# Kernel optimization log

Measured on AMD Instinct MI355X. Metric: run time of the kernel, lower is better.

Reference implementation:

```python
import jax, jax.numpy as jnp
import numpy as np

C, H, W = 96, 128, 128
D_EMB, D_HID = 2, 16


def setup_inputs() -> dict:
    key = jax.random.key(0)
    k1, k2, k3, k4, k5 = jax.random.split(key, 5)
    x = jax.random.normal(k1, (16, C, H, W), dtype=jnp.float32)
    # MLP params: Linear(d_emb, d_hidden) -> ReLU -> Linear(d_hidden, hidden_size)
    W1 = jax.random.normal(k2, (D_EMB, D_HID), dtype=jnp.float32) / np.sqrt(D_EMB)
    b1 = jax.random.normal(k3, (D_HID,), dtype=jnp.float32) * 0.01
    W2 = jax.random.normal(k4, (D_HID, C), dtype=jnp.float32) / np.sqrt(D_HID)
    b2 = jax.random.normal(k5, (C,), dtype=jnp.float32) * 0.01
    return {"x": x, "W1": W1, "b1": b1, "W2": W2, "b2": b2}


def reference(x, W1, b1, W2, b2):
    B, Cc, Hh, Ww = x.shape
    # positional grid (y/H, x/W) in [0,1], shape [H, W, 2]
    gy, gx = jnp.meshgrid(jnp.linspace(0.0, 1.0, Hh), jnp.linspace(0.0, 1.0, Ww), indexing="ij")
    pe = jnp.stack([gy, gx], axis=-1).reshape(-1, 2)  # [H*W, 2]
    hid = jax.nn.relu(pe @ W1 + b1)                   # [H*W, d_hidden]
    k = (hid @ W2 + b2).T.reshape(Cc, Hh, Ww)         # [C, H, W]
    fh, fw = 2 * Hh, 2 * Ww
    k_f = jnp.fft.rfft2(k, s=(fh, fw))                # [C, fh, fw//2+1]
    x_f = jnp.fft.rfft2(x, s=(fh, fw))                # [B, C, fh, fw//2+1]
    # torch: rfft2 norm='backward' (unscaled) + irfft2 norm='forward' (unscaled)
    # => net factor of fh*fw, replicated faithfully via norm='forward'.
    y = jnp.fft.irfft2(x_f * k_f[None], s=(fh, fw), norm="forward")
    y = y[..., :Hh, :Ww]
    return y + x  # residual=True, gelu=False
```

## Files before the change

kernel.cpp:

```cpp
#include <hip/hip_runtime.h>
#include <hip/hip_fp16.h>

#define TWO_PI 6.283185307179586f
#define PI_F   3.14159265358979f

#define HH 128
#define WW 128
#define FN 256
#define NF 129
#define CC 96
#define BB 16

#define SCL_DN 0.0009765625f
#define SCL_UP 1024.0f

typedef unsigned int uint2v __attribute__((ext_vector_type(2)));
typedef __fp16 half2v __attribute__((ext_vector_type(2)));

__device__ __forceinline__ float2 cmul(float2 a, float2 b){
  return make_float2(a.x*b.x - a.y*b.y, a.x*b.y + a.y*b.x);
}
__device__ __forceinline__ float2 cmulc(float2 a, float2 b){
  return make_float2(a.x*b.x + a.y*b.y, a.x*b.y - a.y*b.x);
}
__device__ __forceinline__ float2 cadd(float2 a, float2 b){ return make_float2(a.x+b.x, a.y+b.y); }
__device__ __forceinline__ float2 csub(float2 a, float2 b){ return make_float2(a.x-b.x, a.y-b.y); }
__device__ __forceinline__ float2 shflx(float2 v, int m){
  float2 r; r.x = __shfl_xor(v.x, m, 64); r.y = __shfl_xor(v.y, m, 64); return r;
}
__device__ __forceinline__ float2 shfli(float2 v, int idx){
  float2 r; r.x = __shfl(v.x, idx, 64); r.y = __shfl(v.y, idx, 64); return r;
}
__device__ __forceinline__ unsigned short f2h(float v){ return __half_as_ushort(__float2half(v)); }
__device__ __forceinline__ float h2f(unsigned short u){ return __half2float(__ushort_as_half(u)); }
__device__ __forceinline__ unsigned pkh2(float a, float b){
  union { half2v h; unsigned u; } cv;
  cv.h = __builtin_amdgcn_cvt_pkrtz(a, b);
  return cv.u;
}
__device__ __forceinline__ float h2lo(unsigned u){ return h2f((unsigned short)(u & 0xffffu)); }
__device__ __forceinline__ float h2hi(unsigned u){ return h2f((unsigned short)(u >> 16)); }

__device__ __forceinline__ void swp32(float2 v, float2& lo, float2& hi){
  uint2v rx = __builtin_amdgcn_permlane32_swap(__float_as_uint(v.x), __float_as_uint(v.x), false, false);
  uint2v ry = __builtin_amdgcn_permlane32_swap(__float_as_uint(v.y), __float_as_uint(v.y), false, false);
  lo = make_float2(__uint_as_float(rx[0]), __uint_as_float(ry[0]));
  hi = make_float2(__uint_as_float(rx[1]), __uint_as_float(ry[1]));
}
__device__ __forceinline__ void swp16(float2 v, float2& lo, float2& hi){
  uint2v rx = __builtin_amdgcn_permlane16_swap(__float_as_uint(v.x), __float_as_uint(v.x), false, false);
  uint2v ry = __builtin_amdgcn_permlane16_swap(__float_as_uint(v.y), __float_as_uint(v.y), false, false);
  lo = make_float2(__uint_as_float(rx[0]), __uint_as_float(ry[0]));
  hi = make_float2(__uint_as_float(rx[1]), __uint_as_float(ry[1]));
}
template<int CTRL>
__device__ __forceinline__ float2 dppx(float2 v){
  float2 r;
  r.x = __uint_as_float((unsigned)__builtin_amdgcn_update_dpp(0, (int)__float_as_uint(v.x), CTRL, 0xF, 0xF, true));
  r.y = __uint_as_float((unsigned)__builtin_amdgcn_update_dpp(0, (int)__float_as_uint(v.y), CTRL, 0xF, 0xF, true));
  return r;
}
#define DPP_XOR1 0xB1
#define DPP_XOR2 0x4E

struct Tw {
  float2 w128a, w128b, w64;
  float2 wc[5];
  float2 wf[5];
  float  sg[5];
  float  sg1;
};

__device__ __forceinline__ void tw_init(Tw& t, int l){
  float s, c;
  sincosf(-TWO_PI * (float)l * (1.0f/256.0f), &s, &c);
  t.w128a = make_float2(c, s);
  t.w128b = make_float2(s, -c);
  t.w64   = make_float2(c*c - s*s, 2.0f*c*s);
  const int hs[5] = {32,16,8,4,2};
#pragma unroll
  for (int i = 0; i < 5; ++i){
    int h = hs[i];
    float ang = -PI_F * (float)(l & (h-1)) / (float)h;
    sincosf(ang, &s, &c);
    t.wc[i] = make_float2(c, s);
    bool dn = (l & h) != 0;
    t.wf[i] = dn ? t.wc[i] : make_float2(1.0f, 0.0f);
    t.sg[i] = dn ? -1.0f : 1.0f;
  }
  t.sg1 = (l & 1) ? -1.0f : 1.0f;
}

#define FX_OTHER(X, OTHER, SG, WF) { \
  float2 o_ = OTHER; float2 s_; \
  s_.x = fmaf(SG, X.x, o_.x); s_.y = fmaf(SG, X.y, o_.y); \
  X = cmul(WF, s_); }
#define FX_LOHI(X, SWPF, SG, WF) { \
  float2 lo_, hi_, s_; SWPF(X, lo_, hi_); \
  s_.x = fmaf(SG, hi_.x, lo_.x); s_.y = fmaf(SG, hi_.y, lo_.y); \
  X = cmul(WF, s_); }
#define IX_LOHI(X, SWPF, SG, WC) { \
  float2 lo_, hi_, m_; SWPF(X, lo_, hi_); \
  m_ = cmulc(WC, hi_); \
  X.x = fmaf(SG, m_.x, lo_.x); X.y = fmaf(SG, m_.y, lo_.y); }
#define IX_OTHER(X, OTHER, UP, SG, WC) { \
  float2 o_ = OTHER; \
  float2 A_ = UP ? X : o_; \
  float2 B_ = UP ? o_ : X; \
  float2 m_ = cmulc(WC, B_); \
  X.x = fmaf(SG, m_.x, A_.x); X.y = fmaf(SG, m_.y, A_.y); }

__device__ __forceinline__ void fft256_fwd_padded(float2& x0, float2& x1,
                                                  float2& x2, float2& x3,
                                                  const Tw& t, int l){
  x2 = cmul(x0, t.w128a);
  x3 = cmul(x1, t.w128b);
  float2 a = x0, b = x1;
  x0 = cadd(a, b); x1 = cmul(csub(a, b), t.w64);
  a = x2; b = x3;
  x2 = cadd(a, b); x3 = cmul(csub(a, b), t.w64);
  FX_LOHI(x0, swp32, t.sg[0], t.wf[0]);
  FX_LOHI(x1, swp32, t.sg[0], t.wf[0]);
  FX_LOHI(x2, swp32, t.sg[0], t.wf[0]);
  FX_LOHI(x3, swp32, t.sg[0], t.wf[0]);
  FX_LOHI(x0, swp16, t.sg[1], t.wf[1]);
  FX_LOHI(x1, swp16, t.sg[1], t.wf[1]);
  FX_LOHI(x2, swp16, t.sg[1], t.wf[1]);
  FX_LOHI(x3, swp16, t.sg[1], t.wf[1]);
  FX_OTHER(x0, shflx(x0, 8), t.sg[2], t.wf[2]);
  FX_OTHER(x1, shflx(x1, 8), t.sg[2], t.wf[2]);
  FX_OTHER(x2, shflx(x2, 8), t.sg[2], t.wf[2]);
  FX_OTHER(x3, shflx(x3, 8), t.sg[2], t.wf[2]);
  FX_OTHER(x0, shflx(x0, 4), t.sg[3], t.wf[3]);
  FX_OTHER(x1, shflx(x1, 4), t.sg[3], t.wf[3]);
  FX_OTHER(x2, shflx(x2, 4), t.sg[3], t.wf[3]);
  FX_OTHER(x3, shflx(x3, 4), t.sg[3], t.wf[3]);
  FX_OTHER(x0, dppx<DPP_XOR2>(x0), t.sg[4], t.wf[4]);
  FX_OTHER(x1, dppx<DPP_XOR2>(x1), t.sg[4], t.wf[4]);
  FX_OTHER(x2, dppx<DPP_XOR2>(x2), t.sg[4], t.wf[4]);
  FX_OTHER(x3, dppx<DPP_XOR2>(x3), t.sg[4], t.wf[4]);
  {
    float2 o;
    o = dppx<DPP_XOR1>(x0); x0.x = fmaf(t.sg1, x0.x, o.x); x0.y = fmaf(t.sg1, x0.y, o.y);
    o = dppx<DPP_XOR1>(x1); x1.x = fmaf(t.sg1, x1.x, o.x); x1.y = fmaf(t.sg1, x1.y, o.y);
    o = dppx<DPP_XOR1>(x2); x2.x = fmaf(t.sg1, x2.x, o.x); x2.y = fmaf(t.sg1, x2.y, o.y);
    o = dppx<DPP_XOR1>(x3); x3.x = fmaf(t.sg1, x3.x, o.x); x3.y = fmaf(t.sg1, x3.y, o.y);
  }
}

__device__ __forceinline__ void fft256_inv_crop(float2& x0, float2& x1,
                                                float2& x2, float2& x3,
                                                const Tw& t, int l){
  {
    float2 o;
    o = dppx<DPP_XOR1>(x0); x0.x = fmaf(t.sg1, x0.x, o.x); x0.y = fmaf(t.sg1, x0.y, o.y);
    o = dppx<DPP_XOR1>(x1); x1.x = fmaf(t.sg1, x1.x, o.x); x1.y = fmaf(t.sg1, x1.y, o.y);
    o = dppx<DPP_XOR1>(x2); x2.x = fmaf(t.sg1, x2.x, o.x); x2.y = fmaf(t.sg1, x2.y, o.y);
    o = dppx<DPP_XOR1>(x3); x3.x = fmaf(t.sg1, x3.x, o.x); x3.y = fmaf(t.sg1, x3.y, o.y);
  }
  {
    bool up = (l & 2) == 0;
    IX_OTHER(x0, dppx<DPP_XOR2>(x0), up, t.sg[4], t.wc[4]);
    IX_OTHER(x1, dppx<DPP_XOR2>(x1), up, t.sg[4], t.wc[4]);
    IX_OTHER(x2, dppx<DPP_XOR2>(x2), up, t.sg[4], t.wc[4]);
    IX_OTHER(x3, dppx<DPP_XOR2>(x3), up, t.sg[4], t.wc[4]);
  }
  {
    bool up = (l & 4) == 0;
    IX_OTHER(x0, shflx(x0, 4), up, t.sg[3], t.wc[3]);
    IX_OTHER(x1, shflx(x1, 4), up, t.sg[3], t.wc[3]);
    IX_OTHER(x2, shflx(x2, 4), up, t.sg[3], t.wc[3]);
    IX_OTHER(x3, shflx(x3, 4), up, t.sg[3], t.wc[3]);
  }
  {
    bool up = (l & 8) == 0;
    IX_OTHER(x0, shflx(x0, 8), up, t.sg[2], t.wc[2]);
    IX_OTHER(x1, shflx(x1, 8), up, t.sg[2], t.wc[2]);
    IX_OTHER(x2, shflx(x2, 8), up, t.sg[2], t.wc[2]);
    IX_OTHER(x3, shflx(x3, 8), up, t.sg[2], t.wc[2]);
  }
  IX_LOHI(x0, swp16, t.sg[1], t.wc[1]);
  IX_LOHI(x1, swp16, t.sg[1], t.wc[1]);
  IX_LOHI(x2, swp16, t.sg[1], t.wc[1]);
  IX_LOHI(x3, swp16, t.sg[1], t.wc[1]);
  IX_LOHI(x0, swp32, t.sg[0], t.wc[0]);
  IX_LOHI(x1, swp32, t.sg[0], t.wc[0]);
  IX_LOHI(x2, swp32, t.sg[0], t.wc[0]);
  IX_LOHI(x3, swp32, t.sg[0], t.wc[0]);
  {
    float2 w = make_float2(t.w64.x, -t.w64.y);
    float2 t0 = cmul(w, x1); x1 = csub(x0, t0); x0 = cadd(x0, t0);
    float2 t1 = cmul(w, x3); x3 = csub(x2, t1); x2 = cadd(x2, t1);
  }
  {
    float2 wa = make_float2(t.w128a.x, -t.w128a.y);
    float2 wb = make_float2(t.w128b.x, -t.w128b.y);
    x0 = cadd(x0, cmul(wa, x2));
    x1 = cadd(x1, cmul(wb, x3));
  }
}


__global__ __launch_bounds__(512) void kprep_col(const float* __restrict__ W1,
                                                 const float* __restrict__ b1,
                                                 const float* __restrict__ W2,
                                                 const float* __restrict__ b2,
                                                 float2* __restrict__ Khat){
  __shared__ float sRe[NF*65];
  __shared__ float sIm[NF*65];
  const int S = 65;
  int t = threadIdx.x, l = t & 63, w = t >> 6;
  int c  = blockIdx.x >> 1;
  int q0B = (blockIdx.x & 1) * 64;
  Tw tw; tw_init(tw, l);
  int r6 = __brev((unsigned)l) >> 26;
  int l63 = l ^ 63;
  int p0 = __brev((unsigned)((64 - r6) & 63)) >> 26;

  float w1y[16], w1x[16], bb1[16], w2r[16];
#pragma unroll
  for (int h = 0; h < 16; ++h){
    w1y[h] = W1[h]; w1x[h] = W1[16+h]; bb1[h] = b1[h];
    w2r[h] = W2[h*CC + c] * 0.25f;
  }
  float bb2 = b2[c] * 0.25f;
  float gy0 = (float)l        * (1.0f/127.0f);
  float gy1 = (float)(l + 64) * (1.0f/127.0f);

#define SEPST32(Z, P, ROW) { \
  sRe[(ROW)*S + qa] = Z.x + P.x; sIm[(ROW)*S + qa] = Z.y - P.y; \
  sRe[(ROW)*S + qb] = Z.y + P.y; sIm[(ROW)*S + qb] = P.x - Z.x; }

  for (int ji = 0; ji < 4; ++ji){
    int jj = w*4 + ji;
    int qa = 2*jj, qb = 2*jj + 1;
    float gxa = (float)(q0B + qa) * (1.0f/127.0f);
    float gxb = (float)(q0B + qb) * (1.0f/127.0f);
    float a0 = bb2, a1 = bb2, bq0 = bb2, bq1 = bb2;
#pragma unroll
    for (int h = 0; h < 16; ++h){
      float hxa = gxa*w1x[h] + bb1[h];
      float hxb = gxb*w1x[h] + bb1[h];
      a0  += fmaxf(gy0*w1y[h] + hxa, 0.0f) * w2r[h];
      a1  += fmaxf(gy1*w1y[h] + hxa, 0.0f) * w2r[h];
      bq0 += fmaxf(gy0*w1y[h] + hxb, 0.0f) * w2r[h];
      bq1 += fmaxf(gy1*w1y[h] + hxb, 0.0f) * w2r[h];
    }
    float2 x0 = make_float2(a0, bq0);
    float2 x1 = make_float2(a1, bq1);
    float2 x2, x3;
    fft256_fwd_padded(x0, x1, x2, x3, tw, l);
    float2 f0p = shfli(x0, p0);
    float2 f2p = shfli(x3, l63);
    float2 f1p = shfli(x1, l63);
    float2 f3p = shfli(x2, l63);
    if (r6 <= 32){ SEPST32(x0, f0p, 4*r6); }
    if (r6 <= 31){
      SEPST32(x2, f2p, 4*r6+1);
      SEPST32(x1, f1p, 4*r6+2);
      SEPST32(x3, f3p, 4*r6+3);
    }
  }
#undef SEPST32
  __syncthreads();
  for (int idx = t; idx < NF*64; idx += 512){
    int u = idx >> 6, qq = idx & 63;
    Khat[((size_t)c*NF + u)*FN + q0B + qq] = make_float2(sRe[u*S+qq], sIm[u*S+qq]);
  }
}

__global__ __launch_bounds__(512) void kprep_row(float2* __restrict__ Khat){
  int t = threadIdx.x, l = t & 63, w = t >> 6;
  int c = blockIdx.x >> 2, part = blockIdx.x & 3;
  Tw tw; tw_init(tw, l);
  for (int j = w; ; j += 8){
    int u = part + 4*j;
    if (u >= NF) break;
    float2* kp = Khat + ((size_t)c*NF + u)*FN;
    float2 x0 = kp[l], x1 = kp[64 + l], x2, x3;
    fft256_fwd_padded(x0, x1, x2, x3, tw, l);
    kp[l] = x0; kp[64 + l] = x1; kp[128 + l] = x2; kp[192 + l] = x3;
  }
}

__global__ __launch_bounds__(512) void fused_conv(const float* __restrict__ x,
                                                  const float2* __restrict__ Khat,
                                                  float* __restrict__ out){
  __shared__ unsigned int PL[131*129];
  const int S = 129;
  int t = threadIdx.x, l = t & 63, w = t >> 6;
  int blk = blockIdx.x;
  int c = blk >> 4, b = blk & 15;
  const float* xp = x   + ((size_t)b*CC + c)*(HH*WW);
  float*       yp = out + ((size_t)b*CC + c)*(HH*WW);
  Tw tw; tw_init(tw, l);
  int r6 = __brev((unsigned)l) >> 26;
  int l63 = l ^ 63;
  int p0 = __brev((unsigned)((64 - r6) & 63)) >> 26;

  for (int i = t; i < HH*WW; i += 512){
    int p = i >> 7, q = i & 127;
    PL[p*S + q] = __float_as_uint(xp[i]);
  }
  __syncthreads();
#define SEPST16(Z, P, ROW) { \
  PL[(ROW)*S + q0]     = pkh2(Z.x + P.x, Z.y - P.y); \
  PL[(ROW)*S + q0 + 1] = pkh2(Z.y + P.y, P.x - Z.x); }

  for (int ji = 0; ji < 8; ++ji){
    int jj = w*8 + ji;
    int q0 = 2*jj;
    unsigned v0a = PL[l*S + q0],        v0b = PL[l*S + q0 + 1];
    unsigned v1a = PL[(l+64)*S + q0],   v1b = PL[(l+64)*S + q0 + 1];
    float2 x0 = make_float2(__uint_as_float(v0a), __uint_as_float(v0b));
    float2 x1 = make_float2(__uint_as_float(v1a), __uint_as_float(v1b));
    float2 x2, x3;
    fft256_fwd_padded(x0, x1, x2, x3, tw, l);
    float2 f0p = shfli(x0, p0);
    float2 f2p = shfli(x3, l63);
    float2 f1p = shfli(x1, l63);
    float2 f3p = shfli(x2, l63);
    if (r6 <= 32){ SEPST16(x0, f0p, r6); }
    if (r6 <= 31){
      SEPST16(x2, f2p, 33+r6);
      SEPST16(x1, f1p, 66+r6);
      SEPST16(x3, f3p, 99+r6);
    }
  }
#undef SEPST16
  __syncthreads();
  for (int k = 0; k < 16; ++k){
    int u = w + 8*k;
    if (w == 0 && k == 0){
      unsigned a0 = PL[l],           a1 = PL[64 + l];
      unsigned c0 = PL[32*S + l],    c1 = PL[32*S + 64 + l];
      float2 x0 = make_float2(h2lo(a0), h2lo(c0));
      float2 x1 = make_float2(h2lo(a1), h2lo(c1));
      float2 x2, x3;
      fft256_fwd_padded(x0, x1, x2, x3, tw, l);
      float2 f0p = shfli(x0, p0);
      float2 f2p = shfli(x3, l63);
      float2 f1p = shfli(x1, l63);
      float2 f3p = shfli(x2, l63);
      const float2* k0p = Khat + (size_t)c*NF*FN;
      const float2* k1p = k0p + (size_t)128*FN;
#define PKMUL(Z, P, OFF) { \
      float2 A2_ = make_float2(Z.x + P.x, Z.y - P.y); \
      float2 B2_ = make_float2(Z.y + P.y, P.x - Z.x); \
      float2 m0_ = cmul(A2_, k0p[OFF]); \
      float2 m1_ = cmul(B2_, k1p[OFF]); \
      Z = make_float2(m0_.x - m1_.y, m0_.y + m1_.x); }
      PKMUL(x0, f0p, l);
      PKMUL(x2, f2p, 128 + l);
      PKMUL(x1, f1p, 64 + l);
      PKMUL(x3, f3p, 192 + l);
#undef PKMUL
      fft256_inv_crop(x0, x1, x2, x3, tw, l);
      const float sc = SCL_DN * 0.5f;
      PL[l]           = pkh2(x0.x * sc, 0.0f);
      PL[32*S + l]    = pkh2(x0.y * sc, 0.0f);
      PL[64 + l]      = pkh2(x1.x * sc, 0.0f);
      PL[32*S + 64+l] = pkh2(x1.y * sc, 0.0f);
    } else {
      int pr = (u >> 2) + 33*(u & 3);
      unsigned ua = PL[pr*S + l];
      unsigned ub = PL[pr*S + 64 + l];
      float2 x0 = make_float2(h2lo(ua), h2hi(ua));
      float2 x1 = make_float2(h2lo(ub), h2hi(ub));
      float2 x2, x3;
      fft256_fwd_padded(x0, x1, x2, x3, tw, l);
      const float2* kp = Khat + ((size_t)c*NF + u)*FN;
      x0 = cmul(x0, kp[l]);
      x1 = cmul(x1, kp[64 + l]);
      x2 = cmul(x2, kp[128 + l]);
      x3 = cmul(x3, kp[192 + l]);
      fft256_inv_crop(x0, x1, x2, x3, tw, l);
      PL[pr*S + l]      = pkh2(x0.x * SCL_DN, x0.y * SCL_DN);
      PL[pr*S + 64 + l] = pkh2(x1.x * SCL_DN, x1.y * SCL_DN);
    }
  }
  __syncthreads();
#define GATHV(X, ROWA, ROWB, COND) { \
  int row_ = (COND) ? (ROWA) : (ROWB); \
  float s_ = (COND) ? -1.0f : 1.0f; \
  unsigned ux_ = PL[row_*S + q0]; \
  unsigned uy_ = PL[row_*S + q0 + 1]; \
  X = make_float2(fmaf(s_, h2hi(uy_), h2lo(ux_)), \
                  fmaf(-s_, h2hi(ux_), h2lo(uy_))); }

  for (int ji = 0; ji < 8; ++ji){
    int jj = w*8 + ji;
    int q0 = 2*jj;
    float2 x0, x1, x2, x3;
    GATHV(x0, r6,    64-r6,  r6 <= 32);
    GATHV(x2, 33+r6, 162-r6, r6 <= 31);
    GATHV(x1, 66+r6, 129-r6, r6 <= 31);
    GATHV(x3, 99+r6, 96-r6,  r6 <= 31);
    fft256_inv_crop(x0, x1, x2, x3, tw, l);
    PL[l*S + q0]          = __float_as_uint(x0.x * SCL_UP);
    PL[l*S + q0 + 1]      = __float_as_uint(x0.y * SCL_UP);
    PL[(l+64)*S + q0]     = __float_as_uint(x1.x * SCL_UP);
    PL[(l+64)*S + q0 + 1] = __float_as_uint(x1.y * SCL_UP);
  }
#undef GATHV
  __syncthreads();
  for (int i = t; i < HH*WW; i += 512){
    int p = i >> 7, q = i & 127;
    yp[i] = __uint_as_float(PL[p*S + q]) + xp[i];
  }
}

extern "C" void kernel_launch(void* const* d_in, const int* in_sizes, int n_in,
                              void* d_out, int out_size, void* d_ws, size_t ws_size,
                              hipStream_t stream) {
  const float* x  = (const float*)d_in[0];
  const float* W1 = (const float*)d_in[1];
  const float* b1 = (const float*)d_in[2];
  const float* W2 = (const float*)d_in[3];
  const float* b2 = (const float*)d_in[4];
  float* out = (float*)d_out;

  float2* Khat = (float2*)d_ws;

  kprep_col<<<CC*2, 512, 0, stream>>>(W1, b1, W2, b2, Khat);
  kprep_row<<<CC*4, 512, 0, stream>>>(Khat);
  fused_conv<<<CC*BB, 512, 0, stream>>>(x, Khat, out);
}
```

Before: 419.6 us.

## Run middle-stage FFTs and spectral multiply in packed half2 arithmetic

Replaces the fp32 FFT-256 forward/inverse butterflies in the middle (column) stage of fused_conv with packed __half2 versions that use pre-split real/diagonal twiddle pairs. The kernel spectrum is pre-scaled and stored as packed half2 pairs in the Khat buffer so the pointwise complex multiply becomes two packed FMAs. The aim is to halve ALU work per butterfly and remove fp16<->fp32 conversions around the shared-memory staging. It costs precision, since whole FFT passes now accumulate in fp16, and it adds extra twiddle registers to the thread state.

```diff
diff --git a/kernel.cpp b/kernel.cpp
--- a/kernel.cpp
+++ b/kernel.cpp
@@ -41,6 +41,16 @@
 __device__ __forceinline__ float h2lo(unsigned u){ return h2f((unsigned short)(u & 0xffffu)); }
 __device__ __forceinline__ float h2hi(unsigned u){ return h2f((unsigned short)(u >> 16)); }
 
+__device__ __forceinline__ unsigned h22u(__half2 h){ union{__half2 h; unsigned u;} c; c.h=h; return c.u; }
+__device__ __forceinline__ __half2 u2h2(unsigned u){ union{unsigned u; __half2 h;} c; c.u=u; return c.h; }
+__device__ __forceinline__ __half2 pk2h(float a, float b){ return u2h2(pkh2(a,b)); }
+__device__ __forceinline__ __half2 swap_h2(__half2 a){
+  unsigned u = h22u(a); return u2h2((u >> 16) | (u << 16));
+}
+__device__ __forceinline__ __half2 cmulW_h2(__half2 s, __half2 wrr, __half2 wdd){
+  return __hfma2(swap_h2(s), wdd, __hmul2(s, wrr));
+}
+
 __device__ __forceinline__ void swp32(float2 v, float2& lo, float2& hi){
   uint2v rx = __builtin_amdgcn_permlane32_swap(__float_as_uint(v.x), __float_as_uint(v.x), false, false);
   uint2v ry = __builtin_amdgcn_permlane32_swap(__float_as_uint(v.y), __float_as_uint(v.y), false, false);
@@ -59,6 +69,10 @@
   r.x = __uint_as_float((unsigned)__builtin_amdgcn_update_dpp(0, (int)__float_as_uint(v.x), CTRL, 0xF, 0xF, true));
   r.y = __uint_as_float((unsigned)__builtin_amdgcn_update_dpp(0, (int)__float_as_uint(v.y), CTRL, 0xF, 0xF, true));
   return r;
+}
+template<int CTRL>
+__device__ __forceinline__ unsigned dppu(unsigned v){
+  return (unsigned)__builtin_amdgcn_update_dpp(0, (int)v, CTRL, 0xF, 0xF, true);
 }
 #define DPP_XOR1 0xB1
 #define DPP_XOR2 0x4E
@@ -200,6 +214,137 @@
   }
 }
 
+struct Tw2 {
+  __half2 war, wad, wbr, wbd, w64r, w64d;
+  __half2 wfr[5], wfd[5];
+  __half2 wcr[5], wcdc[5];
+  __half2 sg2[5], sg12;
+  __half2 w64cr, w64cdc, wacr, wacdc, wbcr, wbcdc;
+};
+
+__device__ __forceinline__ void tw2_init(Tw2& t, int l){
+  float s, c;
+  sincosf(-TWO_PI * (float)l * (1.0f/256.0f), &s, &c);
+  float c2 = c*c - s*s, s2 = 2.0f*c*s;
+  t.war  = pk2h(c, c);    t.wad   = pk2h(-s, s);
+  t.wbr  = pk2h(s, s);    t.wbd   = pk2h(c, -c);
+  t.w64r = pk2h(c2, c2);  t.w64d  = pk2h(-s2, s2);
+  t.wacr = pk2h(c, c);    t.wacdc = pk2h(s, -s);
+  t.wbcr = pk2h(s, s);    t.wbcdc = pk2h(-c, c);
+  t.w64cr = pk2h(c2, c2); t.w64cdc = pk2h(s2, -s2);
+  const int hs[5] = {32,16,8,4,2};
+#pragma unroll
+  for (int i = 0; i < 5; ++i){
+    int h = hs[i];
+    float ang = -PI_F * (float)(l & (h-1)) / (float)h;
+    float si, ci; sincosf(ang, &si, &ci);
+    bool dn = (l & h) != 0;
+    t.wfr[i]  = dn ? pk2h(ci, ci) : pk2h(1.0f, 1.0f);
+    t.wfd[i]  = dn ? pk2h(-si, si) : pk2h(0.0f, 0.0f);
+    t.wcr[i]  = pk2h(ci, ci);
+    t.wcdc[i] = pk2h(si, -si);
+    t.sg2[i]  = dn ? pk2h(-1.0f, -1.0f) : pk2h(1.0f, 1.0f);
+  }
+  t.sg12 = (l & 1) ? pk2h(-1.0f, -1.0f) : pk2h(1.0f, 1.0f);
+}
+
+__device__ __forceinline__ void fft256_fwd_h2(__half2& x0, __half2& x1,
+                                              __half2& x2, __half2& x3,
+                                              const Tw2& t){
+  x2 = cmulW_h2(x0, t.war, t.wad);
+  x3 = cmulW_h2(x1, t.wbr, t.wbd);
+  __half2 a = x0;
+  x0 = __hadd2(a, x1);
+  x1 = cmulW_h2(__hsub2(a, x1), t.w64r, t.w64d);
+  a = x2;
+  x2 = __hadd2(a, x3);
+  x3 = cmulW_h2(__hsub2(a, x3), t.w64r, t.w64d);
+#define FWD_P32(X) { unsigned u_ = h22u(X); \
+  uint2v r_ = __builtin_amdgcn_permlane32_swap(u_, u_, false, false); \
+  __half2 s_ = __hfma2(t.sg2[0], u2h2(r_[1]), u2h2(r_[0])); \
+  X = cmulW_h2(s_, t.wfr[0], t.wfd[0]); }
+  FWD_P32(x0) FWD_P32(x1) FWD_P32(x2) FWD_P32(x3)
+#undef FWD_P32
+#define FWD_P16(X) { unsigned u_ = h22u(X); \
+  uint2v r_ = __builtin_amdgcn_permlane16_swap(u_, u_, false, false); \
+  __half2 s_ = __hfma2(t.sg2[1], u2h2(r_[1]), u2h2(r_[0])); \
+  X = cmulW_h2(s_, t.wfr[1], t.wfd[1]); }
+  FWD_P16(x0) FWD_P16(x1) FWD_P16(x2) FWD_P16(x3)
+#undef FWD_P16
+#define FWD_SH(X, M, I) { unsigned o_ = (unsigned)__shfl_xor((int)h22u(X), M, 64); \
+  __half2 s_ = __hfma2(t.sg2[I], X, u2h2(o_)); \
+  X = cmulW_h2(s_, t.wfr[I], t.wfd[I]); }
+  FWD_SH(x0, 8, 2) FWD_SH(x1, 8, 2) FWD_SH(x2, 8, 2) FWD_SH(x3, 8, 2)
+  FWD_SH(x0, 4, 3) FWD_SH(x1, 4, 3) FWD_SH(x2, 4, 3) FWD_SH(x3, 4, 3)
+#undef FWD_SH
+#define FWD_D2(X) { unsigned o_ = dppu<DPP_XOR2>(h22u(X)); \
+  __half2 s_ = __hfma2(t.sg2[4], X, u2h2(o_)); \
+  X = cmulW_h2(s_, t.wfr[4], t.wfd[4]); }
+  FWD_D2(x0) FWD_D2(x1) FWD_D2(x2) FWD_D2(x3)
+#undef FWD_D2
+#define FWD_D1(X) { unsigned o_ = dppu<DPP_XOR1>(h22u(X)); \
+  X = __hfma2(t.sg12, X, u2h2(o_)); }
+  FWD_D1(x0) FWD_D1(x1) FWD_D1(x2) FWD_D1(x3)
+#undef FWD_D1
+}
+
+__device__ __forceinline__ void fft256_inv_h2(__half2& x0, __half2& x1,
+                                              __half2& x2, __half2& x3,
+                                              const Tw2& t, int l){
+#define INV_D1(X) { unsigned o_ = dppu<DPP_XOR1>(h22u(X)); \
+  X = __hfma2(t.sg12, X, u2h2(o_)); }
+  INV_D1(x0) INV_D1(x1) INV_D1(x2) INV_D1(x3)
+#undef INV_D1
+  {
+    bool up = (l & 2) == 0;
+#define INV_D2(X) { unsigned xu_ = h22u(X); unsigned ou_ = dppu<DPP_XOR2>(xu_); \
+    unsigned Au_ = up ? xu_ : ou_; unsigned Bu_ = up ? ou_ : xu_; \
+    __half2 m_ = cmulW_h2(u2h2(Bu_), t.wcr[4], t.wcdc[4]); \
+    X = __hfma2(t.sg2[4], m_, u2h2(Au_)); }
+    INV_D2(x0) INV_D2(x1) INV_D2(x2) INV_D2(x3)
+#undef INV_D2
+  }
+  {
+    bool up = (l & 4) == 0;
+#define INV_S4(X) { unsigned xu_ = h22u(X); \
+    unsigned ou_ = (unsigned)__shfl_xor((int)xu_, 4, 64); \
+    unsigned Au_ = up ? xu_ : ou_; unsigned Bu_ = up ? ou_ : xu_; \
+    __half2 m_ = cmulW_h2(u2h2(Bu_), t.wcr[3], t.wcdc[3]); \
+    X = __hfma2(t.sg2[3], m_, u2h2(Au_)); }
+    INV_S4(x0) INV_S4(x1) INV_S4(x2) INV_S4(x3)
+#undef INV_S4
+  }
+  {
+    bool up = (l & 8) == 0;
+#define INV_S8(X) { unsigned xu_ = h22u(X); \
+    unsigned ou_ = (unsigned)__shfl_xor((int)xu_, 8, 64); \
+    unsigned Au_ = up ? xu_ : ou_; unsigned Bu_ = up ? ou_ : xu_; \
+    __half2 m_ = cmulW_h2(u2h2(Bu_), t.wcr[2], t.wcdc[2]); \
+    X = __hfma2(t.sg2[2], m_, u2h2(Au_)); }
+    INV_S8(x0) INV_S8(x1) INV_S8(x2) INV_S8(x3)
+#undef INV_S8
+  }
+#define INV_P16(X) { unsigned u_ = h22u(X); \
+  uint2v r_ = __builtin_amdgcn_permlane16_swap(u_, u_, false, false); \
+  __half2 m_ = cmulW_h2(u2h2(r_[1]), t.wcr[1], t.wcdc[1]); \
+  X = __hfma2(t.sg2[1], m_, u2h2(r_[0])); }
+  INV_P16(x0) INV_P16(x1) INV_P16(x2) INV_P16(x3)
+#undef INV_P16
+#define INV_P32(X) { unsigned u_ = h22u(X); \
+  uint2v r_ = __builtin_amdgcn_permlane32_swap(u_, u_, false, false); \
+  __half2 m_ = cmulW_h2(u2h2(r_[1]), t.wcr[0], t.wcdc[0]); \
+  X = __hfma2(t.sg2[0], m_, u2h2(r_[0])); }
+  INV_P32(x0) INV_P32(x1) INV_P32(x2) INV_P32(x3)
+#undef INV_P32
+  {
+    __half2 t0 = cmulW_h2(x1, t.w64cr, t.w64cdc);
+    x1 = __hsub2(x0, t0); x0 = __hadd2(x0, t0);
+    __half2 t1 = cmulW_h2(x3, t.w64cr, t.w64cdc);
+    x3 = __hsub2(x2, t1); x2 = __hadd2(x2, t1);
+    x0 = __hadd2(x0, cmulW_h2(x2, t.wacr, t.wacdc));
+    x1 = __hadd2(x1, cmulW_h2(x3, t.wbcr, t.wbcdc));
+  }
+}
 
 __global__ __launch_bounds__(512) void kprep_col(const float* __restrict__ W1,
                                                  const float* __restrict__ b1,
@@ -279,7 +424,11 @@
     float2* kp = Khat + ((size_t)c*NF + u)*FN;
     float2 x0 = kp[l], x1 = kp[64 + l], x2, x3;
     fft256_fwd_padded(x0, x1, x2, x3, tw, l);
-    kp[l] = x0; kp[64 + l] = x1; kp[128 + l] = x2; kp[192 + l] = x3;
+    uint2* kp2 = (uint2*)kp;
+#define KST(V, X) { float re_ = X.x * SCL_DN, im_ = X.y * SCL_DN; \
+    kp2[V] = make_uint2(pkh2(re_, re_), pkh2(-im_, im_)); }
+    KST(l, x0); KST(64 + l, x1); KST(128 + l, x2); KST(192 + l, x3);
+#undef KST
   }
 }
 
@@ -293,7 +442,8 @@
   int c = blk >> 4, b = blk & 15;
   const float* xp = x   + ((size_t)b*CC + c)*(HH*WW);
   float*       yp = out + ((size_t)b*CC + c)*(HH*WW);
-  Tw tw; tw_init(tw, l);
+  Tw tw;  tw_init(tw, l);
+  Tw2 t2; tw2_init(t2, l);
   int r6 = __brev((unsigned)l) >> 26;
   int l63 = l ^ 63;
   int p0 = __brev((unsigned)((64 - r6) & 63)) >> 26;
@@ -334,49 +484,53 @@
     if (w == 0 && k == 0){
       unsigned a0 = PL[l],           a1 = PL[64 + l];
       unsigned c0 = PL[32*S + l],    c1 = PL[32*S + 64 + l];
-      float2 x0 = make_float2(h2lo(a0), h2lo(c0));
-      float2 x1 = make_float2(h2lo(a1), h2lo(c1));
-      float2 x2, x3;
-      fft256_fwd_padded(x0, x1, x2, x3, tw, l);
-      float2 f0p = shfli(x0, p0);
-      float2 f2p = shfli(x3, l63);
-      float2 f1p = shfli(x1, l63);
-      float2 f3p = shfli(x2, l63);
-      const float2* k0p = Khat + (size_t)c*NF*FN;
-      const float2* k1p = k0p + (size_t)128*FN;
-#define PKMUL(Z, P, OFF) { \
-      float2 A2_ = make_float2(Z.x + P.x, Z.y - P.y); \
-      float2 B2_ = make_float2(Z.y + P.y, P.x - Z.x); \
-      float2 m0_ = cmul(A2_, k0p[OFF]); \
-      float2 m1_ = cmul(B2_, k1p[OFF]); \
-      Z = make_float2(m0_.x - m1_.y, m0_.y + m1_.x); }
-      PKMUL(x0, f0p, l);
-      PKMUL(x2, f2p, 128 + l);
-      PKMUL(x1, f1p, 64 + l);
-      PKMUL(x3, f3p, 192 + l);
-#undef PKMUL
-      fft256_inv_crop(x0, x1, x2, x3, tw, l);
-      const float sc = SCL_DN * 0.5f;
-      PL[l]           = pkh2(x0.x * sc, 0.0f);
-      PL[32*S + l]    = pkh2(x0.y * sc, 0.0f);
-      PL[64 + l]      = pkh2(x1.x * sc, 0.0f);
-      PL[32*S + 64+l] = pkh2(x1.y * sc, 0.0f);
+      __half2 x0 = u2h2((a0 & 0xffffu) | (c0 << 16));
+      __half2 x1 = u2h2((a1 & 0xffffu) | (c1 << 16));
+      __half2 x2, x3;
+      fft256_fwd_h2(x0, x1, x2, x3, t2);
+      __half2 f0p = u2h2((unsigned)__shfl((int)h22u(x0), p0, 64));
+      __half2 f2p = u2h2((unsigned)__shfl((int)h22u(x3), l63, 64));
+      __half2 f1p = u2h2((unsigned)__shfl((int)h22u(x1), l63, 64));
+      __half2 f3p = u2h2((unsigned)__shfl((int)h22u(x2), l63, 64));
+      const uint2* k0p = (const uint2*)(Khat + (size_t)c*NF*FN);
+      const uint2* k1p = (const uint2*)(Khat + ((size_t)c*NF + 128)*FN);
+      const __half2 C1M1 = pk2h(1.0f, -1.0f);
+      const __half2 CM11 = pk2h(-1.0f, 1.0f);
+#define PKM(Z, P, OFF) { \
+      __half2 A2_ = __hfma2(P, C1M1, Z); \
+      __half2 B2_ = __hfma2(swap_h2(Z), C1M1, swap_h2(P)); \
+      uint2 k0_ = k0p[OFF], k1_ = k1p[OFF]; \
+      __half2 m0_ = cmulW_h2(A2_, u2h2(k0_.x), u2h2(k0_.y)); \
+      __half2 m1_ = cmulW_h2(B2_, u2h2(k1_.x), u2h2(k1_.y)); \
+      Z = __hfma2(swap_h2(m1_), CM11, m0_); }
+      PKM(x0, f0p, l);
+      PKM(x2, f2p, 128 + l);
+      PKM(x1, f1p, 64 + l);
+      PKM(x3, f3p, 192 + l);
+#undef PKM
+      fft256_inv_h2(x0, x1, x2, x3, t2, l);
+      const __half2 H05 = pk2h(0.5f, 0.5f);
+      unsigned u0 = h22u(__hmul2(x0, H05));
+      unsigned u1 = h22u(__hmul2(x1, H05));
+      PL[l]             = u0 & 0xffffu;
+      PL[32*S + l]      = u0 >> 16;
+      PL[64 + l]        = u1 & 0xffffu;
+      PL[32*S + 64 + l] = u1 >> 16;
     } else {
       int pr = (u >> 2) + 33*(u & 3);
-      unsigned ua = PL[pr*S + l];
-      unsigned ub = PL[pr*S + 64 + l];
-      float2 x0 = make_float2(h2lo(ua), h2hi(ua));
-      float2 x1 = make_float2(h2lo(ub), h2hi(ub));
-      float2 x2, x3;
-      fft256_fwd_padded(x0, x1, x2, x3, tw, l);
-      const float2* kp = Khat + ((size_t)c*NF + u)*FN;
-      x0 = cmul(x0, kp[l]);
-      x1 = cmul(x1, kp[64 + l]);
-      x2 = cmul(x2, kp[128 + l]);
-      x3 = cmul(x3, kp[192 + l]);
-      fft256_inv_crop(x0, x1, x2, x3, tw, l);
-      PL[pr*S + l]      = pkh2(x0.x * SCL_DN, x0.y * SCL_DN);
-      PL[pr*S + 64 + l] = pkh2(x1.x * SCL_DN, x1.y * SCL_DN);
+      __half2 x0 = u2h2(PL[pr*S + l]);
+      __half2 x1 = u2h2(PL[pr*S + 64 + l]);
+      __half2 x2, x3;
+      fft256_fwd_h2(x0, x1, x2, x3, t2);
+      const uint2* kp = (const uint2*)(Khat + ((size_t)c*NF + u)*FN);
+      uint2 ka = kp[l], kb = kp[64 + l], kc = kp[128 + l], kd = kp[192 + l];
+      x0 = cmulW_h2(x0, u2h2(ka.x), u2h2(ka.y));
+      x1 = cmulW_h2(x1, u2h2(kb.x), u2h2(kb.y));
+      x2 = cmulW_h2(x2, u2h2(kc.x), u2h2(kc.y));
+      x3 = cmulW_h2(x3, u2h2(kd.x), u2h2(kd.y));
+      fft256_inv_h2(x0, x1, x2, x3, t2, l);
+      PL[pr*S + l]      = h22u(x0);
+      PL[pr*S + 64 + l] = h22u(x1);
     }
   }
   __syncthreads();
```

Result: faster. 376.9 us (-10.2%).
